# Kernel optimization log

Measured on AMD Instinct MI355X. Metric: run time of the kernel, lower is better.

The kernel has to match this reference:

```python
import jax, jax.numpy as jnp
import numpy as np

B, T, D = 4, 256, 1024
E, DL, TOPK, H = 16, 64, 2, 4


def setup_inputs() -> dict:
    key = jax.random.key(0)
    ks = jax.random.split(key, 12)
    n = lambda k, s: (0.02 * jax.random.normal(k, s)).astype(jnp.float32)
    return dict(
        x=jax.random.normal(ks[0], (B, T, D), dtype=jnp.float32),
        w_down=n(ks[1], (E * DL, D)),
        pos_embed=n(ks[2], (1, E, DL)),
        gp_w=n(ks[3], (DL, D)), gp_b=jnp.zeros((DL,), jnp.float32),
        attn_in_w=n(ks[4], (3 * DL, DL)), attn_in_b=jnp.zeros((3 * DL,), jnp.float32),
        attn_out_w=n(ks[5], (DL, DL)), attn_out_b=jnp.zeros((DL,), jnp.float32),
        ln_w=jnp.ones((DL,), jnp.float32), ln_b=jnp.zeros((DL,), jnp.float32),
        ls_w=n(ks[6], (1, DL)), ls_b=jnp.zeros((1,), jnp.float32),
        g1_w=n(ks[7], (2 * DL, DL)), g1_b=jnp.zeros((2 * DL,), jnp.float32),
        g2_w=n(ks[8], (E, 2 * DL)), g2_b=jnp.zeros((E,), jnp.float32),
        w_up=n(ks[9], (E, DL, D)),
    )


def reference(x, w_down, pos_embed, gp_w, gp_b, attn_in_w, attn_in_b,
              attn_out_w, attn_out_b, ln_w, ln_b, ls_w, ls_b,
              g1_w, g1_b, g2_w, g2_b, w_up):
    Bq, Tq, Dm = x.shape
    N = Bq * Tq
    xf = x.reshape(N, Dm)
    # per-token per-expert low-rank features [N, E, DL]
    ef = (xf @ w_down.T).reshape(N, E, DL)
    # global context per batch element -> [B, DL]
    gctx = x.mean(axis=1) @ gp_w.T + gp_b
    gtok = jnp.repeat(gctx, Tq, axis=0)[:, None, :]  # [N, 1, DL]
    seq = jnp.concatenate([gtok, ef + pos_embed], axis=1)  # [N, E+1, DL]
    # tiny multihead self-attention over E+1 tokens, eval mode (no dropout)
    qkv = seq @ attn_in_w.T + attn_in_b
    q, k, v = jnp.split(qkv, 3, axis=-1)
    hd = DL // H
    sh = lambda t: t.reshape(N, E + 1, H, hd).transpose(0, 2, 1, 3)
    q, k, v = sh(q), sh(k), sh(v)
    scores = jnp.einsum('nhqd,nhkd->nhqk', q, k) / np.float32(np.sqrt(hd))
    attn = jax.nn.softmax(scores, axis=-1)
    ctx = jnp.einsum('nhqk,nhkd->nhqd', attn, v).transpose(0, 2, 1, 3).reshape(N, E + 1, DL)
    attn_out = ctx @ attn_out_w.T + attn_out_b
    h = attn_out + seq
    mu = h.mean(-1, keepdims=True)
    var = h.var(-1, keepdims=True)
    hn = (h - mu) / jnp.sqrt(var + 1e-5) * ln_w + ln_b
    refined = hn[:, 1:, :]  # drop global token -> [N, E, DL]
    local_logits = (refined @ ls_w.T + ls_b)[..., 0]  # [N, E]
    gb = jax.nn.gelu(gctx @ g1_w.T + g1_b, approximate=False) @ g2_w.T + g2_b  # [B, E]
    logits = local_logits + jnp.repeat(gb, Tq, axis=0)
    probs = jax.nn.softmax(logits, axis=-1)
    tw, ti = jax.lax.top_k(probs, TOPK)
    tw = tw / tw.sum(-1, keepdims=True)
    sel = jnp.take_along_axis(ef, ti[..., None], axis=1)  # [N, K, DL]
    act = jax.nn.gelu(sel, approximate=False)
    # gather per-token expert up-projections and batched vec-mat
    eo = jnp.einsum('nkd,nkdm->nkm', act, w_up[ti])  # [N, K, D]
    out = (eo * tw[..., None]).sum(axis=1).reshape(Bq, Tq, Dm)
    mean_prob = probs.mean(axis=0)
    one_hot = jnp.zeros_like(probs).at[jnp.arange(N)[:, None], ti].set(1.0)
    aux_loss = E * jnp.sum(mean_prob * one_hot.mean(axis=0))
    return out, aux_loss
```

## Files before the change

kernel.cpp:

```cpp
#include <hip/hip_runtime.h>
#include <math.h>

#define NB 4
#define TT 256
#define DMODEL 1024
#define NE 16
#define DLQ 64
#define NH 4
#define HD 16
#define SEQL 17
#define NTOK 1024

static constexpr size_t WS_EF    = 0;
static constexpr size_t WS_AH    = 1048576;
static constexpr size_t WS_AL    = 1572864;
static constexpr size_t WS_BH    = 2097152;
static constexpr size_t WS_BL    = 2621440;
static constexpr size_t WS_P1    = 3145728;
static constexpr size_t WS_ACT   = 4194304;
static constexpr size_t WS_AIWFH = 4259840;
static constexpr size_t WS_AIWFL = 4265984;
static constexpr size_t WS_AOWFH = 4272128;
static constexpr size_t WS_AOWFL = 4274176;
static constexpr size_t WS_PR    = 4308992;
static constexpr size_t WS_TI    = 4325376;
static constexpr size_t WS_GCTX  = 4326400;
static constexpr size_t WS_XPART = 4465664;

typedef __attribute__((ext_vector_type(8))) short short8;
typedef __attribute__((ext_vector_type(4))) float f32x4;

__device__ __forceinline__ float gelu_exact(float x) {
    return 0.5f * x * (1.0f + erff(x * 0.70710678118654752f));
}

__device__ __forceinline__ unsigned short f2bf(float f) {
    unsigned int u = __float_as_uint(f);
    unsigned int r = (u + 0x7fffu + ((u >> 16) & 1u)) >> 16;
    return (unsigned short)r;
}
__device__ __forceinline__ float bf2f(unsigned short h) {
    return __uint_as_float(((unsigned int)h) << 16);
}

#define DPP_ADD(v, ctrl) { int _m = __builtin_amdgcn_update_dpp(0, __float_as_int(v), ctrl, 0xF, 0xF, true); \
                           v += __int_as_float(_m); }
__device__ __forceinline__ float rsum16(float v) {
    DPP_ADD(v, 0x128);
    DPP_ADD(v, 0x124);
    DPP_ADD(v, 0x122);
    DPP_ADD(v, 0x121);
    return v;
}
__device__ __forceinline__ float rsum64(float v) {
    v = rsum16(v);
    v += __shfl_xor(v, 16);
    v += __shfl_xor(v, 32);
    return v;
}

__global__ __launch_bounds__(256) void k_prep(const float* __restrict__ x,
                                              const float* __restrict__ wdn,
                                              const float* __restrict__ aiw,
                                              const float* __restrict__ aow,
                                              float* __restrict__ ws) {
    int bi = blockIdx.x;
    int tid = threadIdx.x;
    if (bi < 1024) {
        int which = bi >> 9;
        int t = (bi & 511) * 256 + tid;
        int row = t >> 7;
        int col0 = (t & 127) * 8;
        const float* src = which ? wdn : x;
        unsigned short* hp = (unsigned short*)(ws + (which ? WS_BH : WS_AH));
        unsigned short* lp = (unsigned short*)(ws + (which ? WS_BL : WS_AL));
        float4 v0 = *(const float4*)(src + (size_t)row * DMODEL + col0);
        float4 v1 = *(const float4*)(src + (size_t)row * DMODEL + col0 + 4);
        float vv[8] = {v0.x, v0.y, v0.z, v0.w, v1.x, v1.y, v1.z, v1.w};
        unsigned short h8[8], l8[8];
#pragma unroll
        for (int j = 0; j < 8; ++j) {
            h8[j] = f2bf(vv[j]);
            l8[j] = f2bf(vv[j] - bf2f(h8[j]));
        }
        int nb = row >> 6, kb = col0 >> 6;
        int st = (row & 63) >> 4;
        int ks = (col0 & 63) >> 5;
        int ln = (row & 15) + (((col0 >> 3) & 3) << 4);
        size_t off = (size_t)(nb * 16 + kb) * 4096 + st * 1024 + ks * 512 + ln * 8;
        *(short8*)(hp + off) = *(short8*)h8;
        *(short8*)(lp + off) = *(short8*)l8;
    } else if (bi == 1024) {
        unsigned short* fh = (unsigned short*)(ws + WS_AIWFH);
        unsigned short* fl = (unsigned short*)(ws + WS_AIWFL);
        for (int idx = tid; idx < 12 * 2 * 64; idx += 256) {
            int nt = idx >> 7, kf = (idx >> 6) & 1, l = idx & 63;
            int row = nt * 16 + (l & 15);
            int k = kf * 32 + ((l >> 4) << 3);
            const float* src = aiw + (size_t)row * DLQ + k;
            unsigned short h8[8], l8[8];
#pragma unroll
            for (int j = 0; j < 8; ++j) {
                h8[j] = f2bf(src[j]);
                l8[j] = f2bf(src[j] - bf2f(h8[j]));
            }
            size_t off = (size_t)(nt * 2 + kf) * 512 + l * 8;
            *(short8*)(fh + off) = *(short8*)h8;
            *(short8*)(fl + off) = *(short8*)l8;
        }
        unsigned short* gh = (unsigned short*)(ws + WS_AOWFH);
        unsigned short* gl = (unsigned short*)(ws + WS_AOWFL);
        for (int idx = tid; idx < 4 * 2 * 64; idx += 256) {
            int nt = idx >> 7, kf = (idx >> 6) & 1, l = idx & 63;
            int row = nt * 16 + (l & 15);
            int k = kf * 32 + ((l >> 4) << 3);
            const float* src = aow + (size_t)row * DLQ + k;
            unsigned short h8[8], l8[8];
#pragma unroll
            for (int j = 0; j < 8; ++j) {
                h8[j] = f2bf(src[j]);
                l8[j] = f2bf(src[j] - bf2f(h8[j]));
            }
            size_t off = (size_t)(nt * 2 + kf) * 512 + l * 8;
            *(short8*)(gh + off) = *(short8*)h8;
            *(short8*)(gl + off) = *(short8*)l8;
        }
    } else {
        int idx = bi - 1025;
        int b = idx >> 3, j = idx & 7;
        const float* xb = x + (size_t)(b * 256 + j * 32) * DMODEL + tid * 4;
        float4 acc = {0.f, 0.f, 0.f, 0.f};
#pragma unroll 8
        for (int r = 0; r < 32; ++r) {
            float4 v = *(const float4*)(xb + (size_t)r * DMODEL);
            acc.x += v.x; acc.y += v.y; acc.z += v.z; acc.w += v.w;
        }
        *(float4*)(ws + WS_XPART + (size_t)idx * DMODEL + tid * 4) = acc;
    }
}

__global__ __launch_bounds__(256) void k_ef_mfma(const float* __restrict__ gp_w,
                                                 const float* __restrict__ gp_b,
                                                 float* __restrict__ ws) {
    __shared__ __attribute__((aligned(16))) unsigned short smem[16384];
    int tid = threadIdx.x;
    int bi = blockIdx.x;

    if (bi >= 512) {
        int q = bi - 512;
        int wv = tid >> 6, l = tid & 63;
        float4 xa[4] = {{0.f,0.f,0.f,0.f},{0.f,0.f,0.f,0.f},
                        {0.f,0.f,0.f,0.f},{0.f,0.f,0.f,0.f}};
        const float* xp = ws + WS_XPART + (size_t)q * 8 * DMODEL + l * 16;
#pragma unroll
        for (int j = 0; j < 8; ++j) {
#pragma unroll
            for (int qq = 0; qq < 4; ++qq) {
                float4 v = *(const float4*)(xp + (size_t)j * DMODEL + qq * 4);
                xa[qq].x += v.x; xa[qq].y += v.y; xa[qq].z += v.z; xa[qq].w += v.w;
            }
        }
        float xm[16];
#pragma unroll
        for (int qq = 0; qq < 4; ++qq) {
            xm[qq * 4 + 0] = xa[qq].x * (1.0f / TT);
            xm[qq * 4 + 1] = xa[qq].y * (1.0f / TT);
            xm[qq * 4 + 2] = xa[qq].z * (1.0f / TT);
            xm[qq * 4 + 3] = xa[qq].w * (1.0f / TT);
        }
#pragma unroll 4
        for (int cq = 0; cq < 16; ++cq) {
            int c = wv * 16 + cq;
            const float* gw = gp_w + (size_t)c * DMODEL + l * 16;
            float s = 0.f;
#pragma unroll
            for (int qq = 0; qq < 4; ++qq) {
                float4 w4 = *(const float4*)(gw + qq * 4);
                s += xm[qq * 4 + 0] * w4.x + xm[qq * 4 + 1] * w4.y +
                     xm[qq * 4 + 2] * w4.z + xm[qq * 4 + 3] * w4.w;
            }
            s = rsum64(s);
            if (l == 0) ws[WS_GCTX + q * DLQ + c] = s + gp_b[c];
        }
        return;
    }

    int xcd = bi & 7;
    int g   = bi >> 3;
    int kz  = g >> 5;
    int rem = g & 31;
    int nb  = (xcd >> 1) * 4 + (rem >> 3);
    int mb  = (xcd & 1) * 8 + (rem & 7);

    const unsigned short* AhP = (const unsigned short*)(ws + WS_AH);
    const unsigned short* AlP = (const unsigned short*)(ws + WS_AL);
    const unsigned short* BhP = (const unsigned short*)(ws + WS_BH);
    const unsigned short* BlP = (const unsigned short*)(ws + WS_BL);
    int w = tid >> 6, l = tid & 63;
    int wn = (w >> 1) * 32, wm = (w & 1) * 32;
    int stA = wn >> 4, stB = wm >> 4;
    f32x4 acc00 = {0.f, 0.f, 0.f, 0.f}, acc01 = acc00, acc10 = acc00, acc11 = acc00;

    for (int it = 0; it < 8; ++it) {
        int kb = kz * 8 + it;
        const char* srcs[4] = {
            (const char*)(AhP + (size_t)(nb * 16 + kb) * 4096),
            (const char*)(AlP + (size_t)(nb * 16 + kb) * 4096),
            (const char*)(BhP + (size_t)(mb * 16 + kb) * 4096),
            (const char*)(BlP + (size_t)(mb * 16 + kb) * 4096)};
#pragma unroll
        for (int p = 0; p < 4; ++p) {
#pragma unroll
            for (int h = 0; h < 2; ++h) {
                __builtin_amdgcn_global_load_lds(
                    (const __attribute__((address_space(1))) void*)(srcs[p] + h * 4096 + tid * 16),
                    (__attribute__((address_space(3))) void*)((char*)smem + p * 8192 + h * 4096 + tid * 16),
                    16, 0, 0);
            }
        }
        __syncthreads();
        const unsigned short* Ah = smem;
        const unsigned short* Al = smem + 4096;
        const unsigned short* Bh = smem + 8192;
        const unsigned short* Bl = smem + 12288;
#pragma unroll
        for (int ks = 0; ks < 2; ++ks) {
            short8 ah0 = *(const short8*)(Ah + (stA + 0) * 1024 + ks * 512 + l * 8);
            short8 ah1 = *(const short8*)(Ah + (stA + 1) * 1024 + ks * 512 + l * 8);
            short8 al0 = *(const short8*)(Al + (stA + 0) * 1024 + ks * 512 + l * 8);
            short8 al1 = *(const short8*)(Al + (stA + 1) * 1024 + ks * 512 + l * 8);
            short8 bh0 = *(const short8*)(Bh + (stB + 0) * 1024 + ks * 512 + l * 8);
            short8 bh1 = *(const short8*)(Bh + (stB + 1) * 1024 + ks * 512 + l * 8);
            short8 bl0 = *(const short8*)(Bl + (stB + 0) * 1024 + ks * 512 + l * 8);
            short8 bl1 = *(const short8*)(Bl + (stB + 1) * 1024 + ks * 512 + l * 8);
            acc00 = __builtin_amdgcn_mfma_f32_16x16x32_bf16(ah0, bh0, acc00, 0, 0, 0);
            acc00 = __builtin_amdgcn_mfma_f32_16x16x32_bf16(al0, bh0, acc00, 0, 0, 0);
            acc00 = __builtin_amdgcn_mfma_f32_16x16x32_bf16(ah0, bl0, acc00, 0, 0, 0);
            acc01 = __builtin_amdgcn_mfma_f32_16x16x32_bf16(ah0, bh1, acc01, 0, 0, 0);
            acc01 = __builtin_amdgcn_mfma_f32_16x16x32_bf16(al0, bh1, acc01, 0, 0, 0);
            acc01 = __builtin_amdgcn_mfma_f32_16x16x32_bf16(ah0, bl1, acc01, 0, 0, 0);
            acc10 = __builtin_amdgcn_mfma_f32_16x16x32_bf16(ah1, bh0, acc10, 0, 0, 0);
            acc10 = __builtin_amdgcn_mfma_f32_16x16x32_bf16(al1, bh0, acc10, 0, 0, 0);
            acc10 = __builtin_amdgcn_mfma_f32_16x16x32_bf16(ah1, bl0, acc10, 0, 0, 0);
            acc11 = __builtin_amdgcn_mfma_f32_16x16x32_bf16(ah1, bh1, acc11, 0, 0, 0);
            acc11 = __builtin_amdgcn_mfma_f32_16x16x32_bf16(al1, bh1, acc11, 0, 0, 0);
            acc11 = __builtin_amdgcn_mfma_f32_16x16x32_bf16(ah1, bl1, acc11, 0, 0, 0);
        }
        __syncthreads();
    }
    int cr = (l >> 4) * 4, cc = l & 15;
    int n0 = nb * 64;
    float* P = ws + (kz == 0 ? WS_EF : WS_P1);
    int m0 = mb * 64;
#pragma unroll
    for (int r = 0; r < 4; ++r) {
        P[(size_t)(n0 + wn + cr + r) * DMODEL + (m0 + wm + cc)]           = acc00[r];
        P[(size_t)(n0 + wn + cr + r) * DMODEL + (m0 + wm + 16 + cc)]      = acc01[r];
        P[(size_t)(n0 + wn + 16 + cr + r) * DMODEL + (m0 + wm + cc)]      = acc10[r];
        P[(size_t)(n0 + wn + 16 + cr + r) * DMODEL + (m0 + wm + 16 + cc)] = acc11[r];
    }
}

__global__ __launch_bounds__(128) void k_attn2(const float* __restrict__ pos_embed,
                                               const float* __restrict__ attn_in_b,
                                               const float* __restrict__ attn_out_b,
                                               const float* __restrict__ ln_w,
                                               const float* __restrict__ ln_b,
                                               const float* __restrict__ ls_w,
                                               const float* __restrict__ ls_b,
                                               const float* __restrict__ g1_w,
                                               const float* __restrict__ g1_b,
                                               const float* __restrict__ g2_w,
                                               const float* __restrict__ g2_b,
                                               float* __restrict__ ws) {
    int n = blockIdx.x;
    int w = threadIdx.x >> 6;
    int l = threadIdx.x & 63;
    int b = n >> 8;

    __shared__ float qkv[SEQL * 200];
    __shared__ __attribute__((aligned(16))) char ubuf[8192];
    __shared__ __attribute__((aligned(16))) unsigned short ctxH[1024];
    __shared__ __attribute__((aligned(16))) unsigned short ctxL[1024];
    __shared__ float lgv_sh[NE];
    __shared__ float hsh[128];
    unsigned short* sH = (unsigned short*)ubuf;
    unsigned short* sL = (unsigned short*)(ubuf + 4096);
    float* ao = (float*)ubuf;

    float seqc[SEQL];
    float gcv = ws[WS_GCTX + b * DLQ + l];
    {
        const float* efp0 = ws + WS_EF + (size_t)n * DMODEL;
        const float* efp1 = ws + WS_P1 + (size_t)n * DMODEL;
#pragma unroll
        for (int i = 0; i < SEQL; ++i) {
            float s = (i == 0) ? gcv
                               : efp0[(i - 1) * DLQ + l] + efp1[(i - 1) * DLQ + l] +
                                 pos_embed[(i - 1) * DLQ + l];
            seqc[i] = s;
            int lo_r = w * 9, hi_r = w * 9 + 8;
            if (i >= lo_r && i <= hi_r && i < SEQL) {
                unsigned short hs = f2bf(s);
                unsigned short lsv = f2bf(s - bf2f(hs));
                int mt = i >> 4;
                int ls = (i & 15) + (((l >> 3) & 3) << 4);
                int kf = l >> 5;
                int j = l & 7;
                size_t off = (size_t)(mt * 2 + kf) * 512 + ls * 8 + j;
                sH[off] = hs;
                sL[off] = lsv;
            }
        }
    }
    __syncthreads();

    {
        const unsigned short* fh = (const unsigned short*)(ws + WS_AIWFH);
        const unsigned short* fl = (const unsigned short*)(ws + WS_AIWFL);
        f32x4 acc[6][2];
#pragma unroll
        for (int t = 0; t < 6; ++t)
#pragma unroll
            for (int m = 0; m < 2; ++m) acc[t][m] = (f32x4){0.f, 0.f, 0.f, 0.f};
#pragma unroll
        for (int kf = 0; kf < 2; ++kf) {
            short8 ah0 = *(const short8*)(sH + (0 * 2 + kf) * 512 + l * 8);
            short8 ah1 = *(const short8*)(sH + (1 * 2 + kf) * 512 + l * 8);
            short8 al0 = *(const short8*)(sL + (0 * 2 + kf) * 512 + l * 8);
            short8 al1 = *(const short8*)(sL + (1 * 2 + kf) * 512 + l * 8);
#pragma unroll
            for (int t = 0; t < 6; ++t) {
                int nt = w * 6 + t;
                short8 bh = *(const short8*)(fh + (size_t)(nt * 2 + kf) * 512 + l * 8);
                short8 bl = *(const short8*)(fl + (size_t)(nt * 2 + kf) * 512 + l * 8);
                acc[t][0] = __builtin_amdgcn_mfma_f32_16x16x32_bf16(ah0, bh, acc[t][0], 0, 0, 0);
                acc[t][0] = __builtin_amdgcn_mfma_f32_16x16x32_bf16(al0, bh, acc[t][0], 0, 0, 0);
                acc[t][0] = __builtin_amdgcn_mfma_f32_16x16x32_bf16(ah0, bl, acc[t][0], 0, 0, 0);
                acc[t][1] = __builtin_amdgcn_mfma_f32_16x16x32_bf16(ah1, bh, acc[t][1], 0, 0, 0);
                acc[t][1] = __builtin_amdgcn_mfma_f32_16x16x32_bf16(al1, bh, acc[t][1], 0, 0, 0);
                acc[t][1] = __builtin_amdgcn_mfma_f32_16x16x32_bf16(ah1, bl, acc[t][1], 0, 0, 0);
            }
        }
#pragma unroll
        for (int t = 0; t < 6; ++t) {
            int col = (w * 6 + t) * 16 + (l & 15);
            float bias = attn_in_b[col];
#pragma unroll
            for (int r = 0; r < 4; ++r) {
                int row = (l >> 4) * 4 + r;
                qkv[row * 200 + col] = acc[t][0][r] + bias;
            }
            if ((l >> 4) == 0) qkv[16 * 200 + col] = acc[t][1][0] + bias;
        }
    }
    __syncthreads();

    {
        int g = l >> 4;
        float kc[SEQL], vc[SEQL];
#pragma unroll
        for (int j = 0; j < SEQL; ++j) {
            kc[j] = qkv[j * 200 + 64 + g * 16 + (l & 15)];
            vc[j] = qkv[j * 200 + 128 + l];
        }
        for (int i = w * 8 + 1; i <= w * 8 + 8; ++i) {
            float qi = qkv[i * 200 + g * 16 + (l & 15)];
            float sj[SEQL];
#pragma unroll
            for (int j = 0; j < SEQL; ++j) {
                sj[j] = rsum16(qi * kc[j]) * 0.25f;
            }
            float m = sj[0];
#pragma unroll
            for (int j = 1; j < SEQL; ++j) m = fmaxf(m, sj[j]);
            float ssum = 0.f;
#pragma unroll
            for (int j = 0; j < SEQL; ++j) { sj[j] = __expf(sj[j] - m); ssum += sj[j]; }
            float inv = 1.f / ssum;
            float c = 0.f;
#pragma unroll
            for (int j = 0; j < SEQL; ++j) c += sj[j] * vc[j];
            c *= inv;
            unsigned short ch = f2bf(c);
            unsigned short cl = f2bf(c - bf2f(ch));
            int ls = ((i - 1) & 15) + (((l >> 3) & 3) << 4);
            int kf = l >> 5;
            int j2 = l & 7;
            size_t off = (size_t)kf * 512 + ls * 8 + j2;
            ctxH[off] = ch;
            ctxL[off] = cl;
        }
    }
    __syncthreads();

    {
        const unsigned short* gh = (const unsigned short*)(ws + WS_AOWFH);
        const unsigned short* gl = (const unsigned short*)(ws + WS_AOWFL);
        f32x4 acc[2];
        acc[0] = (f32x4){0.f, 0.f, 0.f, 0.f};
        acc[1] = acc[0];
#pragma unroll
        for (int kf = 0; kf < 2; ++kf) {
            short8 ah = *(const short8*)(ctxH + kf * 512 + l * 8);
            short8 al = *(const short8*)(ctxL + kf * 512 + l * 8);
#pragma unroll
            for (int t = 0; t < 2; ++t) {
                int nt = w * 2 + t;
                short8 bh = *(const short8*)(gh + (size_t)(nt * 2 + kf) * 512 + l * 8);
                short8 bl = *(const short8*)(gl + (size_t)(nt * 2 + kf) * 512 + l * 8);
                acc[t] = __builtin_amdgcn_mfma_f32_16x16x32_bf16(ah, bh, acc[t], 0, 0, 0);
                acc[t] = __builtin_amdgcn_mfma_f32_16x16x32_bf16(al, bh, acc[t], 0, 0, 0);
                acc[t] = __builtin_amdgcn_mfma_f32_16x16x32_bf16(ah, bl, acc[t], 0, 0, 0);
            }
        }
        __syncthreads();
#pragma unroll
        for (int t = 0; t < 2; ++t) {
            int col = (w * 2 + t) * 16 + (l & 15);
            float bias = attn_out_b[col];
#pragma unroll
            for (int r = 0; r < 4; ++r) {
                int row = (l >> 4) * 4 + r;
                ao[row * 72 + col] = acc[t][r] + bias;
            }
        }
    }
    __syncthreads();

    {
#pragma unroll 4
        for (int r = 0; r < 64; ++r) {
            int row = w * 64 + r;
            float s = rsum64(gcv * g1_w[(size_t)row * DLQ + l]);
            if (l == r) hsh[row] = s + g1_b[row];
        }
    }
    __syncthreads();
    float gbv[8];
    {
        float h0 = gelu_exact(hsh[2 * l]);
        float h1 = gelu_exact(hsh[2 * l + 1]);
#pragma unroll
        for (int oo = 0; oo < 8; ++oo) {
            int o = w * 8 + oo;
            gbv[oo] = rsum64(h0 * g2_w[(size_t)o * 128 + 2 * l] +
                             h1 * g2_w[(size_t)o * 128 + 2 * l + 1]) + g2_b[o];
        }
    }

    float rs[SEQL];
#pragma unroll
    for (int i = 1; i < SEQL; ++i) rs[i] = seqc[i] + ao[(i - 1) * 72 + l];

    float c1 = ln_w[l] * ls_w[l];
    float c1sum = rsum64(c1);
    float c0sum = rsum64(ln_b[l] * ls_w[l]);
    float lsb0 = ls_b[0];
#pragma unroll
    for (int ee = 0; ee < 8; ++ee) {
        int e = w * 8 + ee;
        float x = rs[e + 1];
        float s1 = rsum64(x);
        float s2 = rsum64(x * x);
        float s3 = rsum64(x * c1);
        float mu = s1 * (1.0f / DLQ);
        float var = s2 * (1.0f / DLQ) - mu * mu;
        float rstd = rsqrtf(var + 1e-5f);
        float lgv = rstd * (s3 - mu * c1sum) + c0sum + lsb0 + gbv[ee];
        if (l == 0) lgv_sh[e] = lgv;
    }
    __syncthreads();

    if (w == 0) {
        float p[NE];
        float lgv[NE];
#pragma unroll
        for (int e = 0; e < NE; ++e) lgv[e] = lgv_sh[e];
        float m = lgv[0];
#pragma unroll
        for (int e = 1; e < NE; ++e) m = fmaxf(m, lgv[e]);
        float ssum = 0.f;
#pragma unroll
        for (int e = 0; e < NE; ++e) { p[e] = __expf(lgv[e] - m); ssum += p[e]; }
        float inv = 1.f / ssum;
#pragma unroll
        for (int e = 0; e < NE; ++e) p[e] *= inv;
        int t0 = 0; float b0 = p[0];
#pragma unroll
        for (int e = 1; e < NE; ++e) if (p[e] > b0) { b0 = p[e]; t0 = e; }
        int t1 = -1; float b1 = -1.f;
#pragma unroll
        for (int e = 0; e < NE; ++e) if (e != t0 && p[e] > b1) { b1 = p[e]; t1 = e; }

        float sw = b0 + b1;
        float tw0 = b0 / sw, tw1 = b1 / sw;
        unsigned short* actp = (unsigned short*)(ws + WS_ACT);
        float efv0 = ws[WS_EF + (size_t)n * DMODEL + t0 * DLQ + l] +
                     ws[WS_P1 + (size_t)n * DMODEL + t0 * DLQ + l];
        float efv1 = ws[WS_EF + (size_t)n * DMODEL + t1 * DLQ + l] +
                     ws[WS_P1 + (size_t)n * DMODEL + t1 * DLQ + l];
        actp[(size_t)(n * 2 + 0) * 64 + l] = f2bf(gelu_exact(efv0) * tw0);
        actp[(size_t)(n * 2 + 1) * 64 + l] = f2bf(gelu_exact(efv1) * tw1);
        if (l == 0) {
#pragma unroll
            for (int e = 0; e < NE; ++e) ws[WS_PR + (size_t)n * NE + e] = p[e];
            ((int*)(ws + WS_TI))[n] = t0 | (t1 << 8);
        }
    }
}

__global__ __launch_bounds__(256) void k_moe_gemm(const float* __restrict__ w_up,
                                                  float* __restrict__ ws,
                                                  float* __restrict__ out) {
    __shared__ int lst[2048];
    __shared__ int lcnt;
    __shared__ float wsum[4][NE];
    __shared__ int hist[NE];
    int tid = threadIdx.x;
    int wv = tid >> 6, l = tid & 63;

    if (blockIdx.x == NE) {
        if (blockIdx.y != 0) return;
        if (tid < NE) hist[tid] = 0;
        __syncthreads();
        {
            const int* tip = (const int*)(ws + WS_TI);
#pragma unroll
            for (int c = 0; c < 4; ++c) {
                int pk = tip[tid * 4 + c];
                atomicAdd(&hist[pk & 0xff], 1);
                atomicAdd(&hist[(pk >> 8) & 0xff], 1);
            }
        }
        float p[NE];
#pragma unroll
        for (int e = 0; e < NE; ++e) p[e] = 0.f;
        const float* pr = ws + WS_PR + (size_t)tid * 64;
#pragma unroll
        for (int r = 0; r < 4; ++r)
#pragma unroll
            for (int q = 0; q < 4; ++q) {
                float4 v = *(const float4*)(pr + r * 16 + q * 4);
                p[q * 4 + 0] += v.x; p[q * 4 + 1] += v.y;
                p[q * 4 + 2] += v.z; p[q * 4 + 3] += v.w;
            }
#pragma unroll
        for (int e = 0; e < NE; ++e) p[e] = rsum64(p[e]);
        if (l == 0) {
#pragma unroll
            for (int e = 0; e < NE; ++e) wsum[wv][e] = p[e];
        }
        __syncthreads();
        if (tid == 0) {
            float s = 0.f;
#pragma unroll
            for (int e = 0; e < NE; ++e) {
                float sp = wsum[0][e] + wsum[1][e] + wsum[2][e] + wsum[3][e];
                s += sp * (float)hist[e];
            }
            out[(size_t)NTOK * DMODEL] = (float)NE * s / ((float)NTOK * (float)NTOK);
        }
        return;
    }

    int e = blockIdx.x, ct = blockIdx.y;
    if (tid == 0) lcnt = 0;
    __syncthreads();
    {
        const int* tip = (const int*)(ws + WS_TI);
#pragma unroll
        for (int c = 0; c < 4; ++c) {
            int tok = wv * 256 + c * 64 + l;
            int pk = tip[tok];
            bool m1 = ((pk >> 8) & 0xff) == e;
            bool m = ((pk & 0xff) == e) || m1;
            unsigned long long mask = __ballot(m);
            int base = 0;
            if (l == 0 && mask) base = atomicAdd(&lcnt, __popcll(mask));
            base = __shfl(base, 0);
            if (m) {
                int pos = base + __popcll(mask & ((1ull << l) - 1ull));
                lst[pos] = tok * 2 + (m1 ? 1 : 0);
            }
        }
    }
    __syncthreads();
    int cnt = lcnt;
    if (cnt == 0) return;

    int col = ct * 64 + wv * 16 + (l & 15);
    int kb = (l >> 4) * 8;
    const float* wue = w_up + (size_t)e * DLQ * DMODEL + col;
    unsigned short b0v[8], b1v[8];
#pragma unroll
    for (int j = 0; j < 8; ++j) {
        b0v[j] = f2bf(wue[(size_t)(kb + j) * DMODEL]);
        b1v[j] = f2bf(wue[(size_t)(kb + 32 + j) * DMODEL]);
    }
    short8 bf0 = *(short8*)b0v;
    short8 bf1 = *(short8*)b1v;

    const unsigned short* actp = (const unsigned short*)(ws + WS_ACT);
    int cr = (l >> 4) * 4;

    for (int mt = 0; mt < cnt; mt += 16) {
        int row = mt + (l & 15);
        short8 a0 = {0, 0, 0, 0, 0, 0, 0, 0};
        short8 a1 = {0, 0, 0, 0, 0, 0, 0, 0};
        if (row < cnt) {
            int pk = lst[row];
            a0 = *(const short8*)(actp + (size_t)pk * 64 + kb);
            a1 = *(const short8*)(actp + (size_t)pk * 64 + 32 + kb);
        }
        f32x4 acc = {0.f, 0.f, 0.f, 0.f};
        acc = __builtin_amdgcn_mfma_f32_16x16x32_bf16(a0, bf0, acc, 0, 0, 0);
        acc = __builtin_amdgcn_mfma_f32_16x16x32_bf16(a1, bf1, acc, 0, 0, 0);
#pragma unroll
        for (int r = 0; r < 4; ++r) {
            int rr = mt + cr + r;
            if (rr < cnt) {
                int pk = lst[rr];
                atomicAdd(&out[(size_t)(pk >> 1) * DMODEL + col], acc[r]);
            }
        }
    }
}

extern "C" void kernel_launch(void* const* d_in, const int* in_sizes, int n_in,
                              void* d_out, int out_size, void* d_ws, size_t ws_size,
                              hipStream_t stream) {
    const float* x          = (const float*)d_in[0];
    const float* w_down     = (const float*)d_in[1];
    const float* pos_embed  = (const float*)d_in[2];
    const float* gp_w       = (const float*)d_in[3];
    const float* gp_b       = (const float*)d_in[4];
    const float* attn_in_w  = (const float*)d_in[5];
    const float* attn_in_b  = (const float*)d_in[6];
    const float* attn_out_w = (const float*)d_in[7];
    const float* attn_out_b = (const float*)d_in[8];
    const float* ln_w       = (const float*)d_in[9];
    const float* ln_b       = (const float*)d_in[10];
    const float* ls_w       = (const float*)d_in[11];
    const float* ls_b       = (const float*)d_in[12];
    const float* g1_w       = (const float*)d_in[13];
    const float* g1_b       = (const float*)d_in[14];
    const float* g2_w       = (const float*)d_in[15];
    const float* g2_b       = (const float*)d_in[16];
    const float* w_up       = (const float*)d_in[17];
    float* ws  = (float*)d_ws;
    float* out = (float*)d_out;

    hipMemsetAsync(out, 0, (size_t)out_size * sizeof(float), stream);
    k_prep<<<1057, 256, 0, stream>>>(x, w_down, attn_in_w, attn_out_w, ws);
    k_ef_mfma<<<516, 256, 0, stream>>>(gp_w, gp_b, ws);
    k_attn2<<<NTOK, 128, 0, stream>>>(pos_embed, attn_in_b, attn_out_b,
                                      ln_w, ln_b, ls_w, ls_b,
                                      g1_w, g1_b, g2_w, g2_b, ws);
    k_moe_gemm<<<dim3(NE + 1, 16), 256, 0, stream>>>(w_up, ws, out);
}
```

Measured before the change: 185.1 us.

## Fold gate g1 projection into attention QKV MFMA and retile bf16 split prep

Result: faster. 164.2 us (-11.3%).

```diff
diff --git a/kernel.cpp b/kernel.cpp
--- a/kernel.cpp
+++ b/kernel.cpp
@@ -22,6 +22,8 @@
 static constexpr size_t WS_AIWFL = 4265984;
 static constexpr size_t WS_AOWFH = 4272128;
 static constexpr size_t WS_AOWFL = 4274176;
+static constexpr size_t WS_G1FH  = 4276224;
+static constexpr size_t WS_G1FL  = 4280320;
 static constexpr size_t WS_PR    = 4308992;
 static constexpr size_t WS_TI    = 4325376;
 static constexpr size_t WS_GCTX  = 4326400;
@@ -63,34 +65,38 @@
                                               const float* __restrict__ wdn,
                                               const float* __restrict__ aiw,
                                               const float* __restrict__ aow,
+                                              const float* __restrict__ g1w,
                                               float* __restrict__ ws) {
     int bi = blockIdx.x;
     int tid = threadIdx.x;
-    if (bi < 1024) {
-        int which = bi >> 9;
-        int t = (bi & 511) * 256 + tid;
-        int row = t >> 7;
-        int col0 = (t & 127) * 8;
+    if (bi < 512) {
+        int which = bi >> 8;
+        int tix = bi & 255;
+        int nb = tix >> 4, kb = tix & 15;
         const float* src = which ? wdn : x;
         unsigned short* hp = (unsigned short*)(ws + (which ? WS_BH : WS_AH));
         unsigned short* lp = (unsigned short*)(ws + (which ? WS_BL : WS_AL));
-        float4 v0 = *(const float4*)(src + (size_t)row * DMODEL + col0);
-        float4 v1 = *(const float4*)(src + (size_t)row * DMODEL + col0 + 4);
-        float vv[8] = {v0.x, v0.y, v0.z, v0.w, v1.x, v1.y, v1.z, v1.w};
-        unsigned short h8[8], l8[8];
-#pragma unroll
-        for (int j = 0; j < 8; ++j) {
-            h8[j] = f2bf(vv[j]);
-            l8[j] = f2bf(vv[j] - bf2f(h8[j]));
-        }
-        int nb = row >> 6, kb = col0 >> 6;
-        int st = (row & 63) >> 4;
-        int ks = (col0 & 63) >> 5;
-        int ln = (row & 15) + (((col0 >> 3) & 3) << 4);
-        size_t off = (size_t)(nb * 16 + kb) * 4096 + st * 1024 + ks * 512 + ln * 8;
-        *(short8*)(hp + off) = *(short8*)h8;
-        *(short8*)(lp + off) = *(short8*)l8;
-    } else if (bi == 1024) {
+        int w = tid >> 6, ln = tid & 63;
+#pragma unroll
+        for (int h = 0; h < 2; ++h) {
+            int s = w * 2 + h;
+            int st = s >> 1, ks = s & 1;
+            int row = nb * 64 + st * 16 + (ln & 15);
+            int col = kb * 64 + ks * 32 + ((ln >> 4) << 3);
+            float4 v0 = *(const float4*)(src + (size_t)row * DMODEL + col);
+            float4 v1 = *(const float4*)(src + (size_t)row * DMODEL + col + 4);
+            float vv[8] = {v0.x, v0.y, v0.z, v0.w, v1.x, v1.y, v1.z, v1.w};
+            unsigned short h8[8], l8[8];
+#pragma unroll
+            for (int j = 0; j < 8; ++j) {
+                h8[j] = f2bf(vv[j]);
+                l8[j] = f2bf(vv[j] - bf2f(h8[j]));
+            }
+            size_t off = (size_t)tix * 4096 + st * 1024 + ks * 512 + ln * 8;
+            *(short8*)(hp + off) = *(short8*)h8;
+            *(short8*)(lp + off) = *(short8*)l8;
+        }
+    } else if (bi == 512) {
         unsigned short* fh = (unsigned short*)(ws + WS_AIWFH);
         unsigned short* fl = (unsigned short*)(ws + WS_AIWFL);
         for (int idx = tid; idx < 12 * 2 * 64; idx += 256) {
@@ -125,8 +131,25 @@
             *(short8*)(gh + off) = *(short8*)h8;
             *(short8*)(gl + off) = *(short8*)l8;
         }
+        unsigned short* qh = (unsigned short*)(ws + WS_G1FH);
+        unsigned short* ql = (unsigned short*)(ws + WS_G1FL);
+        for (int idx = tid; idx < 8 * 2 * 64; idx += 256) {
+            int nt = idx >> 7, kf = (idx >> 6) & 1, l = idx & 63;
+            int row = nt * 16 + (l & 15);
+            int k = kf * 32 + ((l >> 4) << 3);
+            const float* src = g1w + (size_t)row * DLQ + k;
+            unsigned short h8[8], l8[8];
+#pragma unroll
+            for (int j = 0; j < 8; ++j) {
+                h8[j] = f2bf(src[j]);
+                l8[j] = f2bf(src[j] - bf2f(h8[j]));
+            }
+            size_t off = (size_t)(nt * 2 + kf) * 512 + l * 8;
+            *(short8*)(qh + off) = *(short8*)h8;
+            *(short8*)(ql + off) = *(short8*)l8;
+        }
     } else {
-        int idx = bi - 1025;
+        int idx = bi - 513;
         int b = idx >> 3, j = idx & 7;
         const float* xb = x + (size_t)(b * 256 + j * 32) * DMODEL + tid * 4;
         float4 acc = {0.f, 0.f, 0.f, 0.f};
@@ -268,7 +291,6 @@
                                                const float* __restrict__ ln_b,
                                                const float* __restrict__ ls_w,
                                                const float* __restrict__ ls_b,
-                                               const float* __restrict__ g1_w,
                                                const float* __restrict__ g1_b,
                                                const float* __restrict__ g2_w,
                                                const float* __restrict__ g2_b,
@@ -318,11 +340,16 @@
     {
         const unsigned short* fh = (const unsigned short*)(ws + WS_AIWFH);
         const unsigned short* fl = (const unsigned short*)(ws + WS_AIWFL);
+        const unsigned short* qh = (const unsigned short*)(ws + WS_G1FH);
+        const unsigned short* ql = (const unsigned short*)(ws + WS_G1FL);
         f32x4 acc[6][2];
+        f32x4 accg[4];
 #pragma unroll
         for (int t = 0; t < 6; ++t)
 #pragma unroll
             for (int m = 0; m < 2; ++m) acc[t][m] = (f32x4){0.f, 0.f, 0.f, 0.f};
+#pragma unroll
+        for (int t = 0; t < 4; ++t) accg[t] = (f32x4){0.f, 0.f, 0.f, 0.f};
 #pragma unroll
         for (int kf = 0; kf < 2; ++kf) {
             short8 ah0 = *(const short8*)(sH + (0 * 2 + kf) * 512 + l * 8);
@@ -341,6 +368,15 @@
                 acc[t][1] = __builtin_amdgcn_mfma_f32_16x16x32_bf16(al1, bh, acc[t][1], 0, 0, 0);
                 acc[t][1] = __builtin_amdgcn_mfma_f32_16x16x32_bf16(ah1, bl, acc[t][1], 0, 0, 0);
             }
+#pragma unroll
+            for (int t = 0; t < 4; ++t) {
+                int nt = w * 4 + t;
+                short8 bh = *(const short8*)(qh + (size_t)(nt * 2 + kf) * 512 + l * 8);
+                short8 bl = *(const short8*)(ql + (size_t)(nt * 2 + kf) * 512 + l * 8);
+                accg[t] = __builtin_amdgcn_mfma_f32_16x16x32_bf16(ah0, bh, accg[t], 0, 0, 0);
+                accg[t] = __builtin_amdgcn_mfma_f32_16x16x32_bf16(al0, bh, accg[t], 0, 0, 0);
+                accg[t] = __builtin_amdgcn_mfma_f32_16x16x32_bf16(ah0, bl, accg[t], 0, 0, 0);
+            }
         }
 #pragma unroll
         for (int t = 0; t < 6; ++t) {
@@ -352,6 +388,11 @@
                 qkv[row * 200 + col] = acc[t][0][r] + bias;
             }
             if ((l >> 4) == 0) qkv[16 * 200 + col] = acc[t][1][0] + bias;
+        }
+#pragma unroll
+        for (int t = 0; t < 4; ++t) {
+            int col = (w * 4 + t) * 16 + (l & 15);
+            if ((l >> 4) == 0) hsh[col] = accg[t][0] + g1_b[col];
         }
     }
     __syncthreads();
@@ -428,15 +469,6 @@
     }
     __syncthreads();
 
-    {
-#pragma unroll 4
-        for (int r = 0; r < 64; ++r) {
-            int row = w * 64 + r;
-            float s = rsum64(gcv * g1_w[(size_t)row * DLQ + l]);
-            if (l == r) hsh[row] = s + g1_b[row];
-        }
-    }
-    __syncthreads();
     float gbv[8];
     {
         float h0 = gelu_exact(hsh[2 * l]);
@@ -652,10 +684,10 @@
     float* out = (float*)d_out;
 
     hipMemsetAsync(out, 0, (size_t)out_size * sizeof(float), stream);
-    k_prep<<<1057, 256, 0, stream>>>(x, w_down, attn_in_w, attn_out_w, ws);
+    k_prep<<<545, 256, 0, stream>>>(x, w_down, attn_in_w, attn_out_w, g1_w, ws);
     k_ef_mfma<<<516, 256, 0, stream>>>(gp_w, gp_b, ws);
     k_attn2<<<NTOK, 128, 0, stream>>>(pos_embed, attn_in_b, attn_out_b,
                                       ln_w, ln_b, ls_w, ls_b,
-                                      g1_w, g1_b, g2_w, g2_b, ws);
+                                      g1_b, g2_w, g2_b, ws);
     k_moe_gemm<<<dim3(NE + 1, 16), 256, 0, stream>>>(w_up, ws, out);
 }
```
